# Performance work log

Measured on AMD Instinct MI355X. Metric: run time of the kernel, lower is better.

Reference implementation:

```python
import jax, jax.numpy as jnp
import numpy as np

B, NPB, F = 8, 8192, 64          # clouds, points/cloud, feature dim
RATIO, R, K, C = 0.25, 0.1, 32, 128
M = int(NPB * RATIO)             # 2048 sampled points per cloud


def setup_inputs() -> dict:
    key = jax.random.key(0)
    k1, k2, k3, k4 = jax.random.split(key, 4)
    x = jax.random.normal(k1, (B * NPB, F), dtype=jnp.float32)
    pos = jax.random.uniform(k2, (B * NPB, 3), dtype=jnp.float32)
    batch = (jnp.arange(B * NPB) // NPB).astype(jnp.int32)
    W1 = jax.random.normal(k3, (F + 3, C), dtype=jnp.float32) * (1.0 / np.sqrt(F + 3))
    b1 = jax.random.normal(k4, (C,), dtype=jnp.float32) * 0.01
    return {"x": x, "pos": pos, "batch": batch, "W1": W1, "b1": b1}


def _fps(pos_b):
    # Farthest point sampling on one cloud [NPB,3] -> [M] indices.
    # Deterministic start at index 0 (random_start=False, eval mode).
    dmin0 = jnp.full((NPB,), jnp.inf, dtype=pos_b.dtype)
    def step(carry, _):
        dmin, last = carry
        d = jnp.sum((pos_b - pos_b[last]) ** 2, axis=-1)
        dmin = jnp.minimum(dmin, d)
        nxt = jnp.argmax(dmin).astype(jnp.int32)
        return (dmin, nxt), last
    (_, _), idx = jax.lax.scan(step, (dmin0, jnp.int32(0)), None, length=M)
    return idx


def reference(x, pos, batch, W1, b1):
    posb = pos.reshape(B, NPB, 3)
    xb = x.reshape(B, NPB, F)

    samp = jax.vmap(_fps)(posb)                                   # [B,M] per-cloud idx
    qpos = jnp.take_along_axis(posb, samp[..., None], axis=1)     # [B,M,3]

    # radius ball query: up to K nearest within R (self always included, d=0)
    d2 = jnp.sum((qpos[:, :, None, :] - posb[:, None, :, :]) ** 2, axis=-1)  # [B,M,NPB]
    score = jnp.where(d2 <= R * R, -d2, -jnp.inf)
    vals, nbr = jax.lax.top_k(score, K)                           # [B,M,K]
    valid = vals > -jnp.inf

    flat = nbr.reshape(B, M * K)
    nbr_pos = jnp.take_along_axis(posb, flat[..., None], axis=1).reshape(B, M, K, 3)
    nbr_x = jnp.take_along_axis(xb, flat[..., None], axis=1).reshape(B, M, K, F)

    # PointNet conv: MLP on [x_j, pos_j - pos_i], max-aggregate over neighbors
    msg_in = jnp.concatenate([nbr_x, nbr_pos - qpos[:, :, None, :]], axis=-1)  # [B,M,K,F+3]
    h = jax.nn.relu(jnp.einsum('bmkf,fc->bmkc', msg_in, W1) + b1)
    h = jnp.where(valid[..., None], h, -jnp.inf)
    out = jnp.max(h, axis=2)                                      # [B,M,C]

    idx_global = (samp + (jnp.arange(B, dtype=jnp.int32) * NPB)[:, None]).reshape(-1)
    return (out.reshape(B * M, C),
            qpos.reshape(B * M, 3),
            jnp.take(batch, idx_global),
            idx_global)
```

## Files before the change

kernel.cpp:

```cpp
#include <hip/hip_runtime.h>

#define NPB 8192
#define NB 8
#define MQ 2048
#define FD 64
#define KN 32
#define CD 128
#define NQ (NB*MQ)
#define CAP 512
#define NCB 248
#define NUNITS (NCB*4)
#define UPC (NUNITS/NB)
#define QITERS ((MQ + UPC - 1) / UPC)
#define PSTRIDE 16

typedef unsigned long long ull;
typedef float v2f __attribute__((ext_vector_type(2)));

#define LDS_BARRIER() asm volatile("s_waitcnt lgkmcnt(0)\n\ts_barrier" ::: "memory")

__device__ __forceinline__ float dist2(float ax, float ay, float az,
                                       float bx, float by, float bz) {
    float dx = __fsub_rn(ax, bx);
    float dy = __fsub_rn(ay, by);
    float dz = __fsub_rn(az, bz);
    return __fadd_rn(__fadd_rn(__fmul_rn(dx, dx), __fmul_rn(dy, dy)), __fmul_rn(dz, dz));
}

__device__ __forceinline__ ull dpp_max_u64(ull key) {
#define DPP_STEP(CTRL)                                                          \
    {                                                                           \
        int lo = (int)(unsigned)key, hi = (int)(key >> 32);                     \
        int lo2 = __builtin_amdgcn_update_dpp(0, lo, CTRL, 0xf, 0xf, false);    \
        int hi2 = __builtin_amdgcn_update_dpp(0, hi, CTRL, 0xf, 0xf, false);    \
        ull o = ((ull)(unsigned)hi2 << 32) | (unsigned)lo2;                     \
        if (o > key) key = o;                                                   \
    }
    DPP_STEP(0x111)
    DPP_STEP(0x112)
    DPP_STEP(0x114)
    DPP_STEP(0x118)
    DPP_STEP(0x142)
    DPP_STEP(0x143)
#undef DPP_STEP
    return key;
}

struct FpsSM {
    float2 sxy[NPB];
    float sz[NPB];
    unsigned skeys[NPB];
    __align__(16) ull part[2][8];
};
struct UnitSM {
    float msg[KN][68];
    ull buf[CAP];
    int nb[KN];
    int scnt;
    int pad;
};
union SMU {
    FpsSM f;
    UnitSM u[4];
};

__global__ __launch_bounds__(512) void mega_kernel(const float* __restrict__ xin,
                                                   const float* __restrict__ pos,
                                                   const float* __restrict__ W1,
                                                   const float* __restrict__ b1,
                                                   int* __restrict__ samp,
                                                   int* __restrict__ progress,
                                                   float* __restrict__ out) {
    __shared__ SMU sm;
    const int tid = threadIdx.x;

    if (blockIdx.x < NB) {
        const int b = blockIdx.x;
        const int wv = tid >> 6, lane = tid & 63;
        const float* p0 = pos + (size_t)b * NPB * 3;

        for (int i = tid; i < NPB; i += 512) {
            float x = p0[i * 3 + 0];
            float y = p0[i * 3 + 1];
            float z = p0[i * 3 + 2];
            sm.f.sxy[i] = make_float2(x, y);
            sm.f.sz[i] = z;
            unsigned cx = (unsigned)min(7, max(0, (int)(x * 8.0f)));
            unsigned cy = (unsigned)min(7, max(0, (int)(y * 8.0f)));
            unsigned cz = (unsigned)min(7, max(0, (int)(z * 8.0f)));
            unsigned m = (cx & 1) | ((cy & 1) << 1) | ((cz & 1) << 2)
                       | ((cx & 2) << 2) | ((cy & 2) << 3) | ((cz & 2) << 4)
                       | ((cx & 4) << 4) | ((cy & 4) << 5) | ((cz & 4) << 6);
            sm.f.skeys[i] = (m << 13) | (unsigned)i;
        }
        __syncthreads();

        for (unsigned k = 2; k <= NPB; k <<= 1) {
            for (unsigned j = k >> 1; j > 0; j >>= 1) {
                for (unsigned i = tid; i < NPB / 2; i += 512) {
                    unsigned a = ((i & ~(j - 1)) << 1) | (i & (j - 1));
                    unsigned c = a | j;
                    unsigned x = sm.f.skeys[a], y = sm.f.skeys[c];
                    bool up = ((a & k) == 0);
                    if ((x > y) == up) { sm.f.skeys[a] = y; sm.f.skeys[c] = x; }
                }
                __syncthreads();
            }
        }

        const int perm8[8] = {0, 1, 2, 3, 7, 6, 5, 4};
        const unsigned* sp = &sm.f.skeys[perm8[wv] * 1024 + lane * 16];
        v2f px2[8], py2[8], pz2[8], dmin2[8];
        unsigned norig[16];
        const float inf = __builtin_huge_valf();
        float bx0 = inf, bx1 = -inf;
        float by0 = inf, by1 = -inf;
        float bz0 = inf, bz1 = -inf;
        #pragma unroll
        for (int i = 0; i < 8; i++) {
            unsigned o0 = sp[2 * i + 0] & (NPB - 1);
            unsigned o1 = sp[2 * i + 1] & (NPB - 1);
            norig[2 * i + 0] = ~o0;
            norig[2 * i + 1] = ~o1;
            float2 a = sm.f.sxy[o0], c2 = sm.f.sxy[o1];
            float za = sm.f.sz[o0], zc = sm.f.sz[o1];
            px2[i] = (v2f){a.x, c2.x};
            py2[i] = (v2f){a.y, c2.y};
            pz2[i] = (v2f){za, zc};
            dmin2[i] = (v2f){inf, inf};
            bx0 = fminf(bx0, fminf(a.x, c2.x)); bx1 = fmaxf(bx1, fmaxf(a.x, c2.x));
            by0 = fminf(by0, fminf(a.y, c2.y)); by1 = fmaxf(by1, fmaxf(a.y, c2.y));
            bz0 = fminf(bz0, fminf(za, zc));    bz1 = fmaxf(bz1, fmaxf(za, zc));
        }
        ull mykey = ((ull)0x7f800000u << 32);

        if (tid < 8)
            sm.f.part[1][tid] = ((ull)0x7f800000u << 32) | 0xFFFFFFFFu;
        __syncthreads();

        for (int t = 0; t < MQ; t++) {
            const ulonglong2* pp = (const ulonglong2*)sm.f.part[(t - 1) & 1];
            ulonglong2 q0 = pp[0], q1 = pp[1], q2 = pp[2], q3 = pp[3];
            ull m0 = (q0.x > q0.y) ? q0.x : q0.y;
            ull m1 = (q1.x > q1.y) ? q1.x : q1.y;
            ull m2 = (q2.x > q2.y) ? q2.x : q2.y;
            ull m3 = (q3.x > q3.y) ? q3.x : q3.y;
            m0 = (m0 > m1) ? m0 : m1;
            m2 = (m2 > m3) ? m2 : m3;
            ull g = (m0 > m2) ? m0 : m2;
            int last = ((int)(~(unsigned)g)) & (NPB - 1);

            if (tid == 448) {
                samp[b * MQ + t] = last;
                if ((t & 15) == 15)
                    __hip_atomic_store(&progress[b * PSTRIDE], t + 1, __ATOMIC_RELEASE,
                                       __HIP_MEMORY_SCOPE_AGENT);
            }

            float2 lxy = sm.f.sxy[last];
            float lx = lxy.x, ly = lxy.y, lz = sm.f.sz[last];

            float ddx = fmaxf(fmaxf(bx0 - lx, lx - bx1), 0.0f);
            float ddy = fmaxf(fmaxf(by0 - ly, ly - by1), 0.0f);
            float ddz = fmaxf(fmaxf(bz0 - lz, lz - bz1), 0.0f);
            float dlb = ddx * ddx + ddy * ddy + ddz * ddz;
            float cm = __uint_as_float((unsigned)(mykey >> 32));

            if (__fmul_rn(0.999f, dlb) < cm) {
                #pragma clang fp contract(off)
                ull bestk = 0;
                v2f lxv = {lx, lx}, lyv = {ly, ly}, lzv = {lz, lz};
                #pragma unroll
                for (int i = 0; i < 8; i++) {
                    v2f dx = px2[i] - lxv;
                    v2f dy = py2[i] - lyv;
                    v2f dz = pz2[i] - lzv;
                    v2f d2v = (dx * dx + dy * dy) + dz * dz;
                    float d0 = fminf(dmin2[i].x, d2v.x);
                    float d1 = fminf(dmin2[i].y, d2v.y);
                    dmin2[i] = (v2f){d0, d1};
                    ull k0 = ((ull)__float_as_uint(d0) << 32) | norig[2 * i + 0];
                    ull k1 = ((ull)__float_as_uint(d1) << 32) | norig[2 * i + 1];
                    if (k0 > bestk) bestk = k0;
                    if (k1 > bestk) bestk = k1;
                }
                mykey = bestk;
            }
            ull w = dpp_max_u64(mykey);
            if (lane == 63) sm.f.part[t & 1][wv] = w;
            LDS_BARRIER();
        }
        return;
    }

    const int c = blockIdx.x - NB;
    const int unit = tid >> 7;
    const int ut = tid & 127;
    UnitSM& U = sm.u[unit];
    const int g = c * 4 + unit;
    const int b = g & 7;
    const int ui = g >> 3;
    const float RR = (float)(0.1 * 0.1);
    const float* P = pos + (size_t)b * NPB * 3;

    float w[68];
    #pragma unroll
    for (int f = 0; f < 67; f++) w[f] = W1[f * CD + ut];
    w[67] = 0.0f;
    const float bias = b1[ut];

    for (int r = 0; r < QITERS; r++) {
        const int tq = r * UPC + ui;
        const bool active = tq < MQ;
        const int q = (b << 11) + tq;
        int s = 0;
        float qx = 0.f, qy = 0.f, qz = 0.f;

        if (active && ut == 0) {
            while (__hip_atomic_load(&progress[b * PSTRIDE], __ATOMIC_RELAXED,
                                     __HIP_MEMORY_SCOPE_AGENT) < tq + 1) {}
            __builtin_amdgcn_fence(__ATOMIC_ACQUIRE, "agent");
            U.scnt = 0;
        }
        __syncthreads();

        if (active) {
            s = samp[q] & (NPB - 1);
            qx = P[s * 3 + 0]; qy = P[s * 3 + 1]; qz = P[s * 3 + 2];
            for (int p = ut; p < NPB; p += 128) {
                float xx = P[p * 3 + 0];
                float yy = P[p * 3 + 1];
                float zz = P[p * 3 + 2];
                float d2v = dist2(qx, qy, qz, xx, yy, zz);
                if (d2v <= RR) {
                    int slot = atomicAdd(&U.scnt, 1);
                    if (slot < CAP)
                        U.buf[slot] = ((ull)__float_as_uint(d2v) << 32) | (unsigned)p;
                }
            }
        }
        __syncthreads();

        int n = 0, nk = 0;
        if (active) {
            n = U.scnt; if (n > CAP) n = CAP;
            nk = (n < KN) ? n : KN;
        }
        if (active && ut < 64) {
            if (n <= 64) {
                ull key = (ut < n) ? U.buf[ut] : ~0ULL;
                #pragma unroll
                for (int k = 2; k <= 64; k <<= 1) {
                    #pragma unroll
                    for (int j = k >> 1; j > 0; j >>= 1) {
                        ull o = __shfl_xor(key, (unsigned)j, 64);
                        bool ascending = ((ut & k) == 0);
                        bool upper = ((ut & j) != 0);
                        bool keepMin = (ascending != upper);
                        ull mn = (o < key) ? o : key;
                        ull mx = (o < key) ? key : o;
                        key = keepMin ? mn : mx;
                    }
                }
                if (ut < nk) U.nb[ut] = ((int)(unsigned)key) & (NPB - 1);
            } else {
                ull ck[CAP / 64];
                #pragma unroll
                for (int i = 0; i < CAP / 64; i++) {
                    int sl = ut + i * 64;
                    ck[i] = (sl < n) ? U.buf[sl] : ~0ULL;
                }
                for (int rr = 0; rr < nk; rr++) {
                    ull lm = ck[0];
                    int li = 0;
                    #pragma unroll
                    for (int i = 1; i < CAP / 64; i++) {
                        if (ck[i] < lm) { lm = ck[i]; li = i; }
                    }
                    ull gm = lm;
                    #pragma unroll
                    for (int off = 1; off < 64; off <<= 1) {
                        ull o = __shfl_xor(gm, off, 64);
                        gm = (o < gm) ? o : gm;
                    }
                    ull won = __ballot(lm == gm);
                    int wlane = __ffsll((long long)won) - 1;
                    if (ut == wlane) ck[li] = ~0ULL;
                    if (ut == 0) U.nb[rr] = ((int)(unsigned)gm) & (NPB - 1);
                }
            }
        }
        __syncthreads();

        if (active) {
            const int lane64 = ut & 63, half = ut >> 6;
            for (int k = half; k < nk; k += 2) {
                int p = U.nb[k];
                U.msg[k][lane64] = xin[((size_t)(b * NPB + p)) * FD + lane64];
            }
            if (ut < nk) {
                int p = U.nb[ut];
                U.msg[ut][64] = __fsub_rn(P[p * 3 + 0], qx);
                U.msg[ut][65] = __fsub_rn(P[p * 3 + 1], qy);
                U.msg[ut][66] = __fsub_rn(P[p * 3 + 2], qz);
                U.msg[ut][67] = 0.0f;
            }
        }
        __syncthreads();

        if (active) {
            float acc = 0.0f;
            for (int k = 0; k < nk; k++) {
                float s0 = 0.f, s1 = 0.f, s2 = 0.f, s3 = 0.f;
                #pragma unroll
                for (int f4 = 0; f4 < 17; f4++) {
                    float4 mv = *(const float4*)&U.msg[k][f4 * 4];
                    s0 = fmaf(mv.x, w[f4 * 4 + 0], s0);
                    s1 = fmaf(mv.y, w[f4 * 4 + 1], s1);
                    s2 = fmaf(mv.z, w[f4 * 4 + 2], s2);
                    s3 = fmaf(mv.w, w[f4 * 4 + 3], s3);
                }
                float h = (s0 + s1) + (s2 + s3) + bias;
                h = fmaxf(h, 0.0f);
                acc = fmaxf(acc, h);
            }
            out[(size_t)q * CD + ut] = acc;
            if (ut == 0) {
                float* qp = out + (size_t)NQ * CD;
                qp[q * 3 + 0] = qx;
                qp[q * 3 + 1] = qy;
                qp[q * 3 + 2] = qz;
                float* bo = qp + (size_t)NQ * 3;
                bo[q] = (float)b;
                float* io = bo + NQ;
                io[q] = (float)(b * NPB + s);
            }
        }
    }
}

extern "C" void kernel_launch(void* const* d_in, const int* in_sizes, int n_in,
                              void* d_out, int out_size, void* d_ws, size_t ws_size,
                              hipStream_t stream) {
    const float* x   = (const float*)d_in[0];
    const float* pos = (const float*)d_in[1];
    const float* W1  = (const float*)d_in[3];
    const float* b1  = (const float*)d_in[4];
    float* out = (float*)d_out;

    int* samp = (int*)d_ws;
    int* progress = samp + NQ;

    hipMemsetAsync(progress, 0, NB * PSTRIDE * sizeof(int), stream);
    mega_kernel<<<NB + NCB, 512, 0, stream>>>(x, pos, W1, b1, samp, progress, out);
}
```

Baseline: 1.710 ms.

## Replace bitonic sort with counting sort and streamline FPS per-step reduction

Measured after the change: 1.627 ms. 4.8% less time.

```diff
diff --git a/kernel.cpp b/kernel.cpp
--- a/kernel.cpp
+++ b/kernel.cpp
@@ -27,30 +27,53 @@
     return __fadd_rn(__fadd_rn(__fmul_rn(dx, dx), __fmul_rn(dy, dy)), __fmul_rn(dz, dz));
 }
 
+template <int CTRL>
+__device__ __forceinline__ ull dpp_max_u64_step(ull key) {
+    int lo = (int)(unsigned)key, hi = (int)(key >> 32);
+    int lo2 = __builtin_amdgcn_update_dpp(0, lo, CTRL, 0xf, 0xf, false);
+    int hi2 = __builtin_amdgcn_update_dpp(0, hi, CTRL, 0xf, 0xf, false);
+    ull o = ((ull)(unsigned)hi2 << 32) | (unsigned)lo2;
+    return (o > key) ? o : key;
+}
+
 __device__ __forceinline__ ull dpp_max_u64(ull key) {
-#define DPP_STEP(CTRL)                                                          \
-    {                                                                           \
-        int lo = (int)(unsigned)key, hi = (int)(key >> 32);                     \
-        int lo2 = __builtin_amdgcn_update_dpp(0, lo, CTRL, 0xf, 0xf, false);    \
-        int hi2 = __builtin_amdgcn_update_dpp(0, hi, CTRL, 0xf, 0xf, false);    \
-        ull o = ((ull)(unsigned)hi2 << 32) | (unsigned)lo2;                     \
-        if (o > key) key = o;                                                   \
-    }
-    DPP_STEP(0x111)
-    DPP_STEP(0x112)
-    DPP_STEP(0x114)
-    DPP_STEP(0x118)
-    DPP_STEP(0x142)
-    DPP_STEP(0x143)
-#undef DPP_STEP
+    key = dpp_max_u64_step<0x111>(key);
+    key = dpp_max_u64_step<0x112>(key);
+    key = dpp_max_u64_step<0x114>(key);
+    key = dpp_max_u64_step<0x118>(key);
+    key = dpp_max_u64_step<0x142>(key);
+    key = dpp_max_u64_step<0x143>(key);
     return key;
 }
 
+__device__ __forceinline__ ull dpp_max_u64_groups8(ull key) {
+    key = dpp_max_u64_step<0x118>(key);
+    key = dpp_max_u64_step<0x142>(key);
+    key = dpp_max_u64_step<0x143>(key);
+    return key;
+}
+
+__device__ __forceinline__ unsigned morton9(float x, float y, float z) {
+    unsigned cx = (unsigned)min(7, max(0, (int)(x * 8.0f)));
+    unsigned cy = (unsigned)min(7, max(0, (int)(y * 8.0f)));
+    unsigned cz = (unsigned)min(7, max(0, (int)(z * 8.0f)));
+    return (cx & 1) | ((cy & 1) << 1) | ((cz & 1) << 2)
+         | ((cx & 2) << 2) | ((cy & 2) << 3) | ((cz & 2) << 4)
+         | ((cx & 4) << 4) | ((cy & 4) << 5) | ((cz & 4) << 6);
+}
+
+struct FpsSlot {
+    ull key;
+    float x, y, z;
+    float pad[3];
+};
 struct FpsSM {
     float2 sxy[NPB];
     float sz[NPB];
-    unsigned skeys[NPB];
-    __align__(16) ull part[2][8];
+    unsigned sidx[NPB];
+    __align__(16) FpsSlot slot[2][8];
+    unsigned hist[512];
+    unsigned off[512];
 };
 struct UnitSM {
     float msg[KN][68];
@@ -79,37 +102,53 @@
         const int wv = tid >> 6, lane = tid & 63;
         const float* p0 = pos + (size_t)b * NPB * 3;
 
+        sm.f.hist[tid] = 0;
+        __syncthreads();
         for (int i = tid; i < NPB; i += 512) {
             float x = p0[i * 3 + 0];
             float y = p0[i * 3 + 1];
             float z = p0[i * 3 + 2];
             sm.f.sxy[i] = make_float2(x, y);
             sm.f.sz[i] = z;
-            unsigned cx = (unsigned)min(7, max(0, (int)(x * 8.0f)));
-            unsigned cy = (unsigned)min(7, max(0, (int)(y * 8.0f)));
-            unsigned cz = (unsigned)min(7, max(0, (int)(z * 8.0f)));
-            unsigned m = (cx & 1) | ((cy & 1) << 1) | ((cz & 1) << 2)
-                       | ((cx & 2) << 2) | ((cy & 2) << 3) | ((cz & 2) << 4)
-                       | ((cx & 4) << 4) | ((cy & 4) << 5) | ((cz & 4) << 6);
-            sm.f.skeys[i] = (m << 13) | (unsigned)i;
-        }
-        __syncthreads();
-
-        for (unsigned k = 2; k <= NPB; k <<= 1) {
-            for (unsigned j = k >> 1; j > 0; j >>= 1) {
-                for (unsigned i = tid; i < NPB / 2; i += 512) {
-                    unsigned a = ((i & ~(j - 1)) << 1) | (i & (j - 1));
-                    unsigned c = a | j;
-                    unsigned x = sm.f.skeys[a], y = sm.f.skeys[c];
-                    bool up = ((a & k) == 0);
-                    if ((x > y) == up) { sm.f.skeys[a] = y; sm.f.skeys[c] = x; }
-                }
-                __syncthreads();
-            }
-        }
+            atomicAdd(&sm.f.hist[morton9(x, y, z)], 1);
+        }
+        __syncthreads();
+
+        if (tid < 8) {
+            FpsSlot* d = &sm.f.slot[1][tid];
+            d->key = ((ull)0x7f800000u << 32) | 0xFFFFFFFFu;
+            d->x = sm.f.sxy[0].x;
+            d->y = sm.f.sxy[0].y;
+            d->z = sm.f.sz[0];
+        }
+
+        unsigned hval = sm.f.hist[tid];
+        unsigned* src = sm.f.hist;
+        unsigned* dst = sm.f.off;
+        #pragma unroll 1
+        for (int d = 1; d < 512; d <<= 1) {
+            unsigned v = src[tid];
+            if (tid >= d) v += src[tid - d];
+            __syncthreads();
+            dst[tid] = v;
+            __syncthreads();
+            unsigned* tmp = src; src = dst; dst = tmp;
+        }
+        unsigned excl = src[tid] - hval;
+        dst[tid] = excl;
+        unsigned* cursor = dst;
+        __syncthreads();
+
+        for (int i = tid; i < NPB; i += 512) {
+            float2 xy = sm.f.sxy[i];
+            unsigned m = morton9(xy.x, xy.y, sm.f.sz[i]);
+            unsigned p = atomicAdd(&cursor[m], 1);
+            sm.f.sidx[p] = (unsigned)i;
+        }
+        __syncthreads();
 
         const int perm8[8] = {0, 1, 2, 3, 7, 6, 5, 4};
-        const unsigned* sp = &sm.f.skeys[perm8[wv] * 1024 + lane * 16];
+        const unsigned* sp = &sm.f.sidx[perm8[wv] * 1024 + lane * 16];
         v2f px2[8], py2[8], pz2[8], dmin2[8];
         unsigned norig[16];
         const float inf = __builtin_huge_valf();
@@ -118,8 +157,8 @@
         float bz0 = inf, bz1 = -inf;
         #pragma unroll
         for (int i = 0; i < 8; i++) {
-            unsigned o0 = sp[2 * i + 0] & (NPB - 1);
-            unsigned o1 = sp[2 * i + 1] & (NPB - 1);
+            unsigned o0 = sp[2 * i + 0];
+            unsigned o1 = sp[2 * i + 1];
             norig[2 * i + 0] = ~o0;
             norig[2 * i + 1] = ~o1;
             float2 a = sm.f.sxy[o0], c2 = sm.f.sxy[o1];
@@ -133,22 +172,27 @@
             bz0 = fminf(bz0, fminf(za, zc));    bz1 = fmaxf(bz1, fmaxf(za, zc));
         }
         ull mykey = ((ull)0x7f800000u << 32);
-
-        if (tid < 8)
-            sm.f.part[1][tid] = ((ull)0x7f800000u << 32) | 0xFFFFFFFFu;
+        ull cachedkey = 0;
+        float cachedx = 0.f, cachedy = 0.f, cachedz = 0.f;
         __syncthreads();
 
         for (int t = 0; t < MQ; t++) {
-            const ulonglong2* pp = (const ulonglong2*)sm.f.part[(t - 1) & 1];
-            ulonglong2 q0 = pp[0], q1 = pp[1], q2 = pp[2], q3 = pp[3];
-            ull m0 = (q0.x > q0.y) ? q0.x : q0.y;
-            ull m1 = (q1.x > q1.y) ? q1.x : q1.y;
-            ull m2 = (q2.x > q2.y) ? q2.x : q2.y;
-            ull m3 = (q3.x > q3.y) ? q3.x : q3.y;
-            m0 = (m0 > m1) ? m0 : m1;
-            m2 = (m2 > m3) ? m2 : m3;
-            ull g = (m0 > m2) ? m0 : m2;
-            int last = ((int)(~(unsigned)g)) & (NPB - 1);
+            const FpsSlot* srd = &sm.f.slot[(t - 1) & 1][lane >> 3];
+            ulonglong2 rv = *(const ulonglong2*)srd;
+            float gzf = srd->z;
+            ull kg = rv.x;
+            ull kr = dpp_max_u64_groups8(kg);
+            unsigned whi = (unsigned)__builtin_amdgcn_readlane((int)(kr >> 32), 63);
+            unsigned wlo = (unsigned)__builtin_amdgcn_readlane((int)(unsigned)kr, 63);
+            ull wk = ((ull)whi << 32) | wlo;
+            int last = (int)((~wlo) & (NPB - 1));
+            ull iswin = __ballot(kg == wk);
+            int wl = __ffsll((long long)iswin) - 1;
+            int gxi = (int)(unsigned)rv.y;
+            int gyi = (int)(rv.y >> 32);
+            float lx = __int_as_float(__builtin_amdgcn_readlane(gxi, wl));
+            float ly = __int_as_float(__builtin_amdgcn_readlane(gyi, wl));
+            float lz = __int_as_float(__builtin_amdgcn_readlane(__float_as_int(gzf), wl));
 
             if (tid == 448) {
                 samp[b * MQ + t] = last;
@@ -157,37 +201,52 @@
                                        __HIP_MEMORY_SCOPE_AGENT);
             }
 
-            float2 lxy = sm.f.sxy[last];
-            float lx = lxy.x, ly = lxy.y, lz = sm.f.sz[last];
-
             float ddx = fmaxf(fmaxf(bx0 - lx, lx - bx1), 0.0f);
             float ddy = fmaxf(fmaxf(by0 - ly, ly - by1), 0.0f);
             float ddz = fmaxf(fmaxf(bz0 - lz, lz - bz1), 0.0f);
             float dlb = ddx * ddx + ddy * ddy + ddz * ddz;
             float cm = __uint_as_float((unsigned)(mykey >> 32));
-
-            if (__fmul_rn(0.999f, dlb) < cm) {
-                #pragma clang fp contract(off)
-                ull bestk = 0;
-                v2f lxv = {lx, lx}, lyv = {ly, ly}, lzv = {lz, lz};
-                #pragma unroll
-                for (int i = 0; i < 8; i++) {
-                    v2f dx = px2[i] - lxv;
-                    v2f dy = py2[i] - lyv;
-                    v2f dz = pz2[i] - lzv;
-                    v2f d2v = (dx * dx + dy * dy) + dz * dz;
-                    float d0 = fminf(dmin2[i].x, d2v.x);
-                    float d1 = fminf(dmin2[i].y, d2v.y);
-                    dmin2[i] = (v2f){d0, d1};
-                    ull k0 = ((ull)__float_as_uint(d0) << 32) | norig[2 * i + 0];
-                    ull k1 = ((ull)__float_as_uint(d1) << 32) | norig[2 * i + 1];
-                    if (k0 > bestk) bestk = k0;
-                    if (k1 > bestk) bestk = k1;
-                }
-                mykey = bestk;
-            }
-            ull w = dpp_max_u64(mykey);
-            if (lane == 63) sm.f.part[t & 1][wv] = w;
+            bool act = __fmul_rn(0.999f, dlb) < cm;
+
+            if (__any(act)) {
+                if (act) {
+                    #pragma clang fp contract(off)
+                    ull bestk = 0;
+                    #pragma unroll
+                    for (int i = 0; i < 8; i++) {
+                        v2f dx = px2[i] - lx;
+                        v2f dy = py2[i] - ly;
+                        v2f dz = pz2[i] - lz;
+                        v2f d2v = (dx * dx + dy * dy) + dz * dz;
+                        float d0 = fminf(dmin2[i].x, d2v.x);
+                        float d1 = fminf(dmin2[i].y, d2v.y);
+                        dmin2[i] = (v2f){d0, d1};
+                        ull k0 = ((ull)__float_as_uint(d0) << 32) | norig[2 * i + 0];
+                        ull k1 = ((ull)__float_as_uint(d1) << 32) | norig[2 * i + 1];
+                        if (k0 > bestk) bestk = k0;
+                        if (k1 > bestk) bestk = k1;
+                    }
+                    mykey = bestk;
+                }
+                ull w = dpp_max_u64(mykey);
+                unsigned chi = (unsigned)__builtin_amdgcn_readlane((int)(w >> 32), 63);
+                unsigned clo = (unsigned)__builtin_amdgcn_readlane((int)(unsigned)w, 63);
+                cachedkey = ((ull)chi << 32) | clo;
+                int wi = (int)((~clo) & (NPB - 1));
+                float2 cxy = sm.f.sxy[wi];
+                cachedx = cxy.x;
+                cachedy = cxy.y;
+                cachedz = sm.f.sz[wi];
+            }
+            if (lane == 63) {
+                FpsSlot* d = &sm.f.slot[t & 1][wv];
+                ulonglong2 wv2;
+                wv2.x = cachedkey;
+                wv2.y = ((ull)(unsigned)__float_as_int(cachedy) << 32)
+                      | (unsigned)__float_as_int(cachedx);
+                *(ulonglong2*)d = wv2;
+                d->z = cachedz;
+            }
             LDS_BARRIER();
         }
         return;
```
